# Optimization experiments

Hardware: AMD Instinct MI355X
Metric: run time of the kernel (lower is better)

Reference implementation:

```python
import jax, jax.numpy as jnp
import numpy as np

N_NODES = 50000
N_EDGES = 800000
D = 64       # node_in = edge_in = node_out = edge_out
H = 128      # MLP hidden dim


def mlp(x, W1, b1, W2, b2):
    # 2-layer MLP: Linear -> ReLU -> Linear
    return jax.nn.relu(x @ W1 + b1) @ W2 + b2


def setup_inputs() -> dict:
    key = jax.random.key(0)
    ks = jax.random.split(key, 12)
    s = 0.05  # weight init scale
    return {
        "nf": jax.random.normal(ks[0], (N_NODES, D), jnp.float32),
        "ef": jax.random.normal(ks[1], (N_EDGES, D), jnp.float32),
        "We1": jax.random.normal(ks[2], (D + 2 * D, H), jnp.float32) * s,
        "be1": jnp.zeros((H,), jnp.float32),
        "We2": jax.random.normal(ks[3], (H, D), jnp.float32) * s,
        "be2": jnp.zeros((D,), jnp.float32),
        "Wa1": jax.random.normal(ks[4], (D + 2 * D, H), jnp.float32) * s,
        "ba1": jnp.zeros((H,), jnp.float32),
        "Wa2": jax.random.normal(ks[5], (H, 1), jnp.float32) * s,
        "ba2": jnp.zeros((1,), jnp.float32),
        "Wn1": jax.random.normal(ks[6], (D + D, H), jnp.float32) * s,
        "bn1": jnp.zeros((H,), jnp.float32),
        "Wn2": jax.random.normal(ks[7], (H, D), jnp.float32) * s,
        "bn2": jnp.zeros((D,), jnp.float32),
        "src": jax.random.randint(ks[8], (N_EDGES,), 0, N_NODES, jnp.int32),
        "dst": jax.random.randint(ks[9], (N_EDGES,), 0, N_NODES, jnp.int32),
    }


def reference(nf, ef, We1, be1, We2, be2, Wa1, ba1, Wa2, ba2,
              Wn1, bn1, Wn2, bn2, src, dst):
    # --- edge update: gather src/dst node feats, concat, MLP ---
    em_input = jnp.concatenate([ef, nf[src], nf[dst]], axis=-1)  # [E, 3D]
    uef = mlp(em_input, We1, be1, We2, be2)                       # [E, D]

    # --- edge softmax over incoming edges of each dst node ---
    logits = mlp(em_input, Wa1, ba1, Wa2, ba2)[:, 0]              # [E]
    seg_max = jax.ops.segment_max(logits, dst, num_segments=N_NODES)
    e = jnp.exp(logits - seg_max[dst])
    seg_sum = jax.ops.segment_sum(e, dst, num_segments=N_NODES)
    attn = (e / seg_sum[dst])[:, None]                            # [E, 1]

    # --- attention-weighted message, mean-aggregate to dst ---
    msg = uef * attn                                              # [E, D]
    agg = jax.ops.segment_sum(msg, dst, num_segments=N_NODES)     # [N, D]
    cnt = jax.ops.segment_sum(jnp.ones_like(msg[:, 0]), dst, num_segments=N_NODES)
    agg_m = agg / jnp.maximum(cnt, 1.0)[:, None]                  # mean; 0 for isolated nodes

    # --- node update: concat [agg_m, nf], MLP ---
    unf = mlp(jnp.concatenate([agg_m, nf], axis=-1), Wn1, bn1, Wn2, bn2)
    return unf, uef
```

## Files before the change

### kernel.cpp

```cpp
#include <hip/hip_runtime.h>
#include <hip/hip_bf16.h>
#include <cstdint>

#define E_EDGES 800000
#define NN 50000

typedef __attribute__((ext_vector_type(8))) short short8;
typedef __attribute__((ext_vector_type(4))) float f32x4;
typedef __attribute__((ext_vector_type(16))) float f32x16;

#define MFMA32(a,b,c) __builtin_amdgcn_mfma_f32_32x32x16_bf16((a),(b),(c),0,0,0)
#define MFMA16(a,b,c) __builtin_amdgcn_mfma_f32_16x16x32_bf16((a),(b),(c),0,0,0)

#define OFF_WE1T   0u
#define OFF_WA1T   49152u
#define OFF_WE2T   98304u
#define OFF_WN1T   114688u
#define OFF_WN2T   147456u
#define OFF_LOGIT  163840u
#define OFF_SEGMAXU (OFF_LOGIT + E_EDGES*4u)
#define OFF_SEGSUM (OFF_SEGMAXU + NN*4u)
#define OFF_CNTI   (OFF_SEGSUM + NN*4u)
#define OFF_CURSOR (OFF_CNTI + NN*4u)
#define OFF_ROWPTR (OFF_CURSOR + NN*4u)
#define OFF_EIDX   (OFF_ROWPTR + 200064u)
#define OFF_AGG    (OFF_EIDX + E_EDGES*4u)

__device__ __forceinline__ unsigned short bf16s(float f) {
    unsigned u = __float_as_uint(f);
    u = (u + 0x7FFFu + ((u >> 16) & 1u)) >> 16;
    return (unsigned short)u;
}
__device__ __forceinline__ unsigned fkey(float f) {
    unsigned u = __float_as_uint(f);
    return (u & 0x80000000u) ? ~u : (u | 0x80000000u);
}
__device__ __forceinline__ float funkey(unsigned k) {
    unsigned u = (k & 0x80000000u) ? (k & 0x7FFFFFFFu) : ~k;
    return __uint_as_float(u);
}

__global__ void k0_init(const float* __restrict__ We1, const float* __restrict__ Wa1,
                        const float* __restrict__ We2, const float* __restrict__ Wn1,
                        const float* __restrict__ Wn2, char* __restrict__ ws) {
    int idx = blockIdx.x * 256 + threadIdx.x;
    unsigned short* we1t = (unsigned short*)(ws + OFF_WE1T);
    unsigned short* wa1t = (unsigned short*)(ws + OFF_WA1T);
    unsigned short* we2t = (unsigned short*)(ws + OFF_WE2T);
    unsigned short* wn1t = (unsigned short*)(ws + OFF_WN1T);
    unsigned short* wn2t = (unsigned short*)(ws + OFF_WN2T);
    if (idx < 128 * 192) {
        int n = idx / 192, k = idx % 192;
        we1t[idx] = bf16s(We1[k * 128 + n]);
        wa1t[idx] = bf16s(Wa1[k * 128 + n]);
    }
    if (idx < 64 * 128) {
        int n = idx / 128, k = idx % 128;
        we2t[idx] = bf16s(We2[k * 64 + n]);
        wn2t[idx] = bf16s(Wn2[k * 64 + n]);
    }
    if (idx < 128 * 128) {
        int n = idx / 128, k = idx % 128;
        wn1t[idx] = bf16s(Wn1[k * 128 + n]);
    }
}

__global__ __launch_bounds__(256) void khist(const int* __restrict__ dst, char* __restrict__ ws) {
    int e = blockIdx.x * 256 + threadIdx.x;
    if (e >= E_EDGES) return;
    atomicAdd((int*)(ws + OFF_CNTI) + dst[e], 1);
}

__global__ __launch_bounds__(1024) void kscan(char* __restrict__ ws) {
    __shared__ int part[1024];
    const int t = threadIdx.x;
    const int* cnt = (const int*)(ws + OFF_CNTI);
    int* rowptr = (int*)(ws + OFF_ROWPTR);
    const int base0 = t * 49;
    int s = 0;
#pragma unroll 7
    for (int i = 0; i < 49; ++i) { int idx = base0 + i; if (idx < NN) s += cnt[idx]; }
    part[t] = s;
    __syncthreads();
    for (int off = 1; off < 1024; off <<= 1) {
        int v = (t >= off) ? part[t - off] : 0;
        __syncthreads();
        part[t] += v;
        __syncthreads();
    }
    int run = part[t] - s;
    for (int i = 0; i < 49; ++i) {
        int idx = base0 + i;
        if (idx < NN) { rowptr[idx] = run; run += cnt[idx]; }
    }
    if (t == 1023) rowptr[NN] = part[1023];
}

__global__ __launch_bounds__(256, 2) void k1_edge(
    const float* __restrict__ nf, const float* __restrict__ ef,
    const float* __restrict__ be1, const float* __restrict__ be2,
    const float* __restrict__ ba1, const float* __restrict__ Wa2,
    const float* __restrict__ ba2, const int* __restrict__ src,
    const int* __restrict__ dst, char* __restrict__ ws,
    float* __restrict__ uef_out) {
    __shared__ __align__(16) unsigned short sW[2 * 128 * 40];
    __shared__ __align__(16) unsigned short sH[128 * 136];

    const int tid = threadIdx.x;
    const int wv = tid >> 6;
    const int l = tid & 63;
    const int m32 = l & 31;
    const int half = l >> 5;
    const long ebase = (long)blockIdx.x * 128;
    const long erow = ebase + wv * 32 + m32;
    const int sa = src[erow], da = dst[erow];

    const unsigned short* __restrict__ We1T = (const unsigned short*)(ws + OFF_WE1T);
    const unsigned short* __restrict__ Wa1T = (const unsigned short*)(ws + OFF_WA1T);
    const unsigned short* __restrict__ We2T = (const unsigned short*)(ws + OFF_WE2T);

    short8 A[12];
    {
        const float* __restrict__ pe = ef + erow * 64;
        const float* __restrict__ ps = nf + (long)sa * 64;
        const float* __restrict__ pd = nf + (long)da * 64;
#pragma unroll
        for (int seg = 0; seg < 3; ++seg) {
            const float* p = (seg == 0 ? pe : (seg == 1 ? ps : pd));
#pragma unroll
            for (int t = 0; t < 4; ++t) {
                f32x4 v0 = *(const f32x4*)(p + t * 16 + half * 8);
                f32x4 v1 = *(const f32x4*)(p + t * 16 + half * 8 + 4);
                short8 a;
#pragma unroll
                for (int j = 0; j < 4; ++j) {
                    a[j] = (short)bf16s(v0[j]);
                    a[4 + j] = (short)bf16s(v1[j]);
                }
                A[seg * 4 + t] = a;
            }
        }
    }

    f32x16 accE[4], accA[4];
#pragma unroll
    for (int i = 0; i < 4; ++i) {
#pragma unroll
        for (int j = 0; j < 16; ++j) { accE[i][j] = 0.f; accA[i][j] = 0.f; }
    }

#pragma unroll
    for (int kk = 0; kk < 6; ++kk) {
#pragma unroll
        for (int c = 0; c < 4; ++c) {
            int ci = tid + c * 256;
            int mat = ci >> 9;
            int r = (ci >> 2) & 127;
            int c8 = (ci & 3) << 3;
            *(short8*)&sW[mat * 5120 + r * 40 + c8] =
                *(const short8*)((mat ? Wa1T : We1T) + r * 192 + kk * 32 + c8);
        }
        __syncthreads();
#pragma unroll
        for (int ks = 0; ks < 2; ++ks) {
            short8 a = A[kk * 2 + ks];
#pragma unroll
            for (int nt = 0; nt < 4; ++nt) {
                const int bo = (nt * 32 + m32) * 40 + ks * 16 + half * 8;
                short8 b0 = *(const short8*)&sW[bo];
                short8 b1 = *(const short8*)&sW[5120 + bo];
                accE[nt] = MFMA32(a, b0, accE[nt]);
                accA[nt] = MFMA32(a, b1, accA[nt]);
            }
        }
        __syncthreads();
    }

    {
        float ba1v[4], wa2v[4];
#pragma unroll
        for (int nt = 0; nt < 4; ++nt) {
            int cc = nt * 32 + m32;
            ba1v[nt] = ba1[cc];
            wa2v[nt] = Wa2[cc];
        }
        float lg[16];
#pragma unroll
        for (int r = 0; r < 16; ++r) {
            float p = 0.f;
#pragma unroll
            for (int nt = 0; nt < 4; ++nt)
                p += fmaxf(accA[nt][r] + ba1v[nt], 0.f) * wa2v[nt];
            lg[r] = p;
        }
#pragma unroll
        for (int mk = 1; mk < 32; mk <<= 1) {
#pragma unroll
            for (int r = 0; r < 16; ++r) lg[r] += __shfl_xor(lg[r], mk, 64);
        }
        if (m32 == 0) {
            float bb2 = ba2[0];
            float* logits = (float*)(ws + OFF_LOGIT);
            unsigned* segmaxu = (unsigned*)(ws + OFF_SEGMAXU);
#pragma unroll
            for (int r = 0; r < 16; ++r) {
                long er = ebase + wv * 32 + (r & 3) + 8 * (r >> 2) + 4 * half;
                float v = lg[r] + bb2;
                logits[er] = v;
                atomicMax(&segmaxu[dst[er]], fkey(v));
            }
        }
    }

#pragma unroll
    for (int nt = 0; nt < 4; ++nt) {
        int cc = nt * 32 + m32;
        float bb = be1[cc];
#pragma unroll
        for (int r = 0; r < 16; ++r) {
            int rowl = wv * 32 + (r & 3) + 8 * (r >> 2) + 4 * half;
            sH[rowl * 136 + cc] = bf16s(fmaxf(accE[nt][r] + bb, 0.f));
        }
    }
#pragma unroll
    for (int c = 0; c < 4; ++c) {
        int ci = tid + c * 256;
        int r = ci >> 4;
        int c8 = (ci & 15) << 3;
        *(short8*)&sW[r * 136 + c8] = *(const short8*)(We2T + r * 128 + c8);
    }
    __syncthreads();

    f32x16 acc2[2];
#pragma unroll
    for (int i = 0; i < 2; ++i) {
#pragma unroll
        for (int j = 0; j < 16; ++j) acc2[i][j] = 0.f;
    }
#pragma unroll
    for (int s = 0; s < 8; ++s) {
        short8 a2 = *(const short8*)&sH[(wv * 32 + m32) * 136 + s * 16 + half * 8];
#pragma unroll
        for (int nt = 0; nt < 2; ++nt) {
            short8 b = *(const short8*)&sW[(nt * 32 + m32) * 136 + s * 16 + half * 8];
            acc2[nt] = MFMA32(a2, b, acc2[nt]);
        }
    }
#pragma unroll
    for (int nt = 0; nt < 2; ++nt) {
        int cc = nt * 32 + m32;
        float bb = be2[cc];
#pragma unroll
        for (int r = 0; r < 16; ++r) {
            long er = ebase + wv * 32 + (r & 3) + 8 * (r >> 2) + 4 * half;
            uef_out[er * 64 + cc] = acc2[nt][r] + bb;
        }
    }
}

__global__ __launch_bounds__(256) void k2_pass(const int* __restrict__ dst, char* __restrict__ ws) {
    int e = blockIdx.x * 256 + threadIdx.x;
    if (e >= E_EDGES) return;
    float* lexp = (float*)(ws + OFF_LOGIT);
    const unsigned* segmaxu = (const unsigned*)(ws + OFF_SEGMAXU);
    float* segsum = (float*)(ws + OFF_SEGSUM);
    int* cursor = (int*)(ws + OFF_CURSOR);
    const int* rowptr = (const int*)(ws + OFF_ROWPTR);
    int* eidx = (int*)(ws + OFF_EIDX);
    int d = dst[e];
    float ev = __expf(lexp[e] - funkey(segmaxu[d]));
    lexp[e] = ev;
    atomicAdd(&segsum[d], ev);
    int pos = atomicAdd(&cursor[d], 1);
    eidx[rowptr[d] + pos] = e;
}

__global__ __launch_bounds__(256) void k3_gather(char* __restrict__ ws,
                                                 const float* __restrict__ uef) {
    int node = blockIdx.x * 4 + (threadIdx.x >> 6);
    int c = threadIdx.x & 63;
    const int* rowptr = (const int*)(ws + OFF_ROWPTR);
    const int* eidx = (const int*)(ws + OFF_EIDX);
    const float* eexp = (const float*)(ws + OFF_LOGIT);
    const float* segsum = (const float*)(ws + OFF_SEGSUM);
    float* agg = (float*)(ws + OFF_AGG);
    int beg = rowptr[node], end = rowptr[node + 1];
    float acc = 0.f;
    for (int i = beg; i < end; ++i) {
        int e = eidx[i];
        acc += eexp[e] * uef[(long)e * 64 + c];
    }
    float out = 0.f;
    if (end > beg) out = acc / (segsum[node] * (float)(end - beg));
    agg[(long)node * 64 + c] = out;
}

__global__ __launch_bounds__(256) void k4_node(
    const float* __restrict__ nf, const float* __restrict__ bn1,
    const float* __restrict__ bn2, char* __restrict__ ws,
    float* __restrict__ unf_out) {
    __shared__ __align__(16) unsigned short sW[8704];
    __shared__ __align__(16) unsigned short sH[64 * 136];

    const int tid = threadIdx.x;
    const int wv = tid >> 6;
    const int lane = tid & 63;
    const int c16 = lane & 15;
    const int quad = lane >> 4;
    const int nbase = blockIdx.x * 64;
    int node = nbase + wv * 16 + c16;
    int nodec = min(node, NN - 1);

    const float* agg = (const float*)(ws + OFF_AGG);
    const unsigned short* Wn1T = (const unsigned short*)(ws + OFF_WN1T);
    const unsigned short* Wn2T = (const unsigned short*)(ws + OFF_WN2T);
    const float* __restrict__ pa = agg + (long)nodec * 64;
    const float* __restrict__ pn = nf + (long)nodec * 64;

    f32x4 acc[8];
#pragma unroll
    for (int i = 0; i < 8; ++i) acc[i] = (f32x4){0, 0, 0, 0};

#pragma unroll
    for (int kk = 0; kk < 4; ++kk) {
#pragma unroll
        for (int c = 0; c < 2; ++c) {
            int ci = tid + c * 256;
            int r = ci >> 2;
            int c8 = (ci & 3) << 3;
            *(short8*)&sW[r * 40 + c8] = *(const short8*)(Wn1T + r * 128 + kk * 32 + c8);
        }
        __syncthreads();
        const float* p = (kk < 2 ? pa : pn) + (kk & 1) * 32 + quad * 8;
        f32x4 f0 = *(const f32x4*)p;
        f32x4 f1 = *(const f32x4*)(p + 4);
        short8 a;
#pragma unroll
        for (int i = 0; i < 4; ++i) { a[i] = (short)bf16s(f0[i]); a[4 + i] = (short)bf16s(f1[i]); }
#pragma unroll
        for (int nt = 0; nt < 8; ++nt) {
            short8 b = *(const short8*)&sW[(nt * 16 + c16) * 40 + quad * 8];
            acc[nt] = MFMA16(a, b, acc[nt]);
        }
        __syncthreads();
    }

#pragma unroll
    for (int nt = 0; nt < 8; ++nt) {
        int cc = nt * 16 + c16;
        float bb = bn1[cc];
#pragma unroll
        for (int r = 0; r < 4; ++r) {
            float h = fmaxf(acc[nt][r] + bb, 0.f);
            sH[(wv * 16 + quad * 4 + r) * 136 + cc] = bf16s(h);
        }
    }
#pragma unroll
    for (int c = 0; c < 4; ++c) {
        int ci = tid + c * 256;
        int r = ci >> 4;
        int c8 = (ci & 15) << 3;
        *(short8*)&sW[r * 136 + c8] = *(const short8*)(Wn2T + r * 128 + c8);
    }
    __syncthreads();

    f32x4 acc2[4];
#pragma unroll
    for (int i = 0; i < 4; ++i) acc2[i] = (f32x4){0, 0, 0, 0};
#pragma unroll
    for (int kk = 0; kk < 4; ++kk) {
        short8 a2 = *(const short8*)&sH[(wv * 16 + c16) * 136 + kk * 32 + quad * 8];
#pragma unroll
        for (int nt = 0; nt < 4; ++nt) {
            short8 b = *(const short8*)&sW[(nt * 16 + c16) * 136 + kk * 32 + quad * 8];
            acc2[nt] = MFMA16(a2, b, acc2[nt]);
        }
    }
#pragma unroll
    for (int nt = 0; nt < 4; ++nt) {
        int cc = nt * 16 + c16;
        float bb = bn2[cc];
#pragma unroll
        for (int r = 0; r < 4; ++r) {
            int nrow = nbase + wv * 16 + quad * 4 + r;
            if (nrow < NN) unf_out[(long)nrow * 64 + cc] = acc2[nt][r] + bb;
        }
    }
}

extern "C" void kernel_launch(void* const* d_in, const int* in_sizes, int n_in,
                              void* d_out, int out_size, void* d_ws, size_t ws_size,
                              hipStream_t stream) {
    const float* nf  = (const float*)d_in[0];
    const float* ef  = (const float*)d_in[1];
    const float* We1 = (const float*)d_in[2];
    const float* be1 = (const float*)d_in[3];
    const float* We2 = (const float*)d_in[4];
    const float* be2 = (const float*)d_in[5];
    const float* Wa1 = (const float*)d_in[6];
    const float* ba1 = (const float*)d_in[7];
    const float* Wa2 = (const float*)d_in[8];
    const float* ba2 = (const float*)d_in[9];
    const float* Wn1 = (const float*)d_in[10];
    const float* bn1 = (const float*)d_in[11];
    const float* Wn2 = (const float*)d_in[12];
    const float* bn2 = (const float*)d_in[13];
    const int* src = (const int*)d_in[14];
    const int* dst = (const int*)d_in[15];
    char* ws = (char*)d_ws;
    float* unf_out = (float*)d_out;
    float* uef_out = (float*)d_out + (size_t)NN * 64;

    hipMemsetAsync(ws + OFF_SEGMAXU, 0, (size_t)NN * 4 * 4, stream);
    k0_init<<<96, 256, 0, stream>>>(We1, Wa1, We2, Wn1, Wn2, ws);
    khist<<<E_EDGES / 256, 256, 0, stream>>>(dst, ws);
    kscan<<<1, 1024, 0, stream>>>(ws);
    k1_edge<<<E_EDGES / 128, 256, 0, stream>>>(nf, ef, be1, be2, ba1, Wa2, ba2, src, dst, ws, uef_out);
    k2_pass<<<E_EDGES / 256, 256, 0, stream>>>(dst, ws);
    k3_gather<<<NN / 4, 256, 0, stream>>>(ws, uef_out);
    k4_node<<<(NN + 63) / 64, 256, 0, stream>>>(nf, bn1, bn2, ws, unf_out);
}
```

Baseline: 928.8 us.

## Replace CSR build and gather with atomic scatter of weighted messages

Drops the histogram, scan and edge-index bucketing kernels along with the CSR gather. Each edge now atomically adds exp-weighted uef rows straight into the per-node aggregate, plus its segsum and count. The softmax division and mean normalization move into the node kernel as a per-node scale. This removes three launches and the serial single-block scan. In exchange it issues 51.2M float atomics on random destinations and makes the summation order nondeterministic.

```diff
diff --git a/kernel.cpp b/kernel.cpp
--- a/kernel.cpp
+++ b/kernel.cpp
@@ -21,10 +21,7 @@
 #define OFF_SEGMAXU (OFF_LOGIT + E_EDGES*4u)
 #define OFF_SEGSUM (OFF_SEGMAXU + NN*4u)
 #define OFF_CNTI   (OFF_SEGSUM + NN*4u)
-#define OFF_CURSOR (OFF_CNTI + NN*4u)
-#define OFF_ROWPTR (OFF_CURSOR + NN*4u)
-#define OFF_EIDX   (OFF_ROWPTR + 200064u)
-#define OFF_AGG    (OFF_EIDX + E_EDGES*4u)
+#define OFF_AGG    (OFF_CNTI + NN*4u)
 
 __device__ __forceinline__ unsigned short bf16s(float f) {
     unsigned u = __float_as_uint(f);
@@ -65,37 +62,6 @@
     }
 }
 
-__global__ __launch_bounds__(256) void khist(const int* __restrict__ dst, char* __restrict__ ws) {
-    int e = blockIdx.x * 256 + threadIdx.x;
-    if (e >= E_EDGES) return;
-    atomicAdd((int*)(ws + OFF_CNTI) + dst[e], 1);
-}
-
-__global__ __launch_bounds__(1024) void kscan(char* __restrict__ ws) {
-    __shared__ int part[1024];
-    const int t = threadIdx.x;
-    const int* cnt = (const int*)(ws + OFF_CNTI);
-    int* rowptr = (int*)(ws + OFF_ROWPTR);
-    const int base0 = t * 49;
-    int s = 0;
-#pragma unroll 7
-    for (int i = 0; i < 49; ++i) { int idx = base0 + i; if (idx < NN) s += cnt[idx]; }
-    part[t] = s;
-    __syncthreads();
-    for (int off = 1; off < 1024; off <<= 1) {
-        int v = (t >= off) ? part[t - off] : 0;
-        __syncthreads();
-        part[t] += v;
-        __syncthreads();
-    }
-    int run = part[t] - s;
-    for (int i = 0; i < 49; ++i) {
-        int idx = base0 + i;
-        if (idx < NN) { rowptr[idx] = run; run += cnt[idx]; }
-    }
-    if (t == 1023) rowptr[NN] = part[1023];
-}
-
 __global__ __launch_bounds__(256, 2) void k1_edge(
     const float* __restrict__ nf, const float* __restrict__ ef,
     const float* __restrict__ be1, const float* __restrict__ be2,
@@ -258,41 +224,22 @@
     }
 }
 
-__global__ __launch_bounds__(256) void k2_pass(const int* __restrict__ dst, char* __restrict__ ws) {
-    int e = blockIdx.x * 256 + threadIdx.x;
-    if (e >= E_EDGES) return;
-    float* lexp = (float*)(ws + OFF_LOGIT);
+__global__ __launch_bounds__(256) void k2_scatter(const int* __restrict__ dst,
+                                                  char* __restrict__ ws,
+                                                  const float* __restrict__ uef) {
+    const int tid = threadIdx.x;
+    const long e = (long)blockIdx.x * 4 + (tid >> 6);
+    const int c = tid & 63;
+    const float* logits = (const float*)(ws + OFF_LOGIT);
     const unsigned* segmaxu = (const unsigned*)(ws + OFF_SEGMAXU);
     float* segsum = (float*)(ws + OFF_SEGSUM);
-    int* cursor = (int*)(ws + OFF_CURSOR);
-    const int* rowptr = (const int*)(ws + OFF_ROWPTR);
-    int* eidx = (int*)(ws + OFF_EIDX);
-    int d = dst[e];
-    float ev = __expf(lexp[e] - funkey(segmaxu[d]));
-    lexp[e] = ev;
-    atomicAdd(&segsum[d], ev);
-    int pos = atomicAdd(&cursor[d], 1);
-    eidx[rowptr[d] + pos] = e;
-}
-
-__global__ __launch_bounds__(256) void k3_gather(char* __restrict__ ws,
-                                                 const float* __restrict__ uef) {
-    int node = blockIdx.x * 4 + (threadIdx.x >> 6);
-    int c = threadIdx.x & 63;
-    const int* rowptr = (const int*)(ws + OFF_ROWPTR);
-    const int* eidx = (const int*)(ws + OFF_EIDX);
-    const float* eexp = (const float*)(ws + OFF_LOGIT);
-    const float* segsum = (const float*)(ws + OFF_SEGSUM);
+    int* cnti = (int*)(ws + OFF_CNTI);
     float* agg = (float*)(ws + OFF_AGG);
-    int beg = rowptr[node], end = rowptr[node + 1];
-    float acc = 0.f;
-    for (int i = beg; i < end; ++i) {
-        int e = eidx[i];
-        acc += eexp[e] * uef[(long)e * 64 + c];
-    }
-    float out = 0.f;
-    if (end > beg) out = acc / (segsum[node] * (float)(end - beg));
-    agg[(long)node * 64 + c] = out;
+    const int d = dst[e];
+    const float ev = __expf(logits[e] - funkey(segmaxu[d]));
+    if (c == 0) atomicAdd(&segsum[d], ev);
+    if (c == 1) atomicAdd(&cnti[d], 1);
+    atomicAdd(&agg[(long)d * 64 + c], ev * uef[e * 64 + c]);
 }
 
 __global__ __launch_bounds__(256) void k4_node(
@@ -312,10 +259,18 @@
     int nodec = min(node, NN - 1);
 
     const float* agg = (const float*)(ws + OFF_AGG);
+    const float* segsum = (const float*)(ws + OFF_SEGSUM);
+    const int* cnti = (const int*)(ws + OFF_CNTI);
     const unsigned short* Wn1T = (const unsigned short*)(ws + OFF_WN1T);
     const unsigned short* Wn2T = (const unsigned short*)(ws + OFF_WN2T);
     const float* __restrict__ pa = agg + (long)nodec * 64;
     const float* __restrict__ pn = nf + (long)nodec * 64;
+
+    float sc = 0.f;
+    {
+        int ct = cnti[nodec];
+        if (ct > 0) sc = 1.f / (segsum[nodec] * (float)ct);
+    }
 
     f32x4 acc[8];
 #pragma unroll
@@ -332,11 +287,15 @@
         }
         __syncthreads();
         const float* p = (kk < 2 ? pa : pn) + (kk & 1) * 32 + quad * 8;
+        const float m = (kk < 2) ? sc : 1.f;
         f32x4 f0 = *(const f32x4*)p;
         f32x4 f1 = *(const f32x4*)(p + 4);
         short8 a;
 #pragma unroll
-        for (int i = 0; i < 4; ++i) { a[i] = (short)bf16s(f0[i]); a[4 + i] = (short)bf16s(f1[i]); }
+        for (int i = 0; i < 4; ++i) {
+            a[i] = (short)bf16s(f0[i] * m);
+            a[4 + i] = (short)bf16s(f1[i] * m);
+        }
 #pragma unroll
         for (int nt = 0; nt < 8; ++nt) {
             short8 b = *(const short8*)&sW[(nt * 16 + c16) * 40 + quad * 8];
@@ -411,12 +370,9 @@
     float* unf_out = (float*)d_out;
     float* uef_out = (float*)d_out + (size_t)NN * 64;
 
-    hipMemsetAsync(ws + OFF_SEGMAXU, 0, (size_t)NN * 4 * 4, stream);
+    hipMemsetAsync(ws + OFF_SEGMAXU, 0, (size_t)NN * 12 + (size_t)NN * 256, stream);
     k0_init<<<96, 256, 0, stream>>>(We1, Wa1, We2, Wn1, Wn2, ws);
-    khist<<<E_EDGES / 256, 256, 0, stream>>>(dst, ws);
-    kscan<<<1, 1024, 0, stream>>>(ws);
     k1_edge<<<E_EDGES / 128, 256, 0, stream>>>(nf, ef, be1, be2, ba1, Wa2, ba2, src, dst, ws, uef_out);
-    k2_pass<<<E_EDGES / 256, 256, 0, stream>>>(dst, ws);
-    k3_gather<<<NN / 4, 256, 0, stream>>>(ws, uef_out);
+    k2_scatter<<<E_EDGES / 4, 256, 0, stream>>>(dst, ws, uef_out);
     k4_node<<<(NN + 63) / 64, 256, 0, stream>>>(nf, bn1, bn2, ws, unf_out);
 }
```

Result: faster. 858.7 us (-7.5%).
